# Optimization experiments

Measured on AMD Instinct MI355X. Metric: run time of the kernel, lower is better.

The kernel has to match this reference:

```python
import jax, jax.numpy as jnp
import numpy as np


def setup_inputs() -> dict:
    key = jax.random.key(0)
    k1, k2, k3 = jax.random.split(key, 3)
    B, N, Nq, D, Dv = 32, 4096, 8, 64, 64
    return {
        "keys": jax.random.normal(k1, (B, N, D), dtype=jnp.float32),
        "values": jax.random.normal(k2, (B, N, Dv), dtype=jnp.float32),
        "query": jax.random.normal(k3, (B, Nq, D), dtype=jnp.float32),
    }


def reference(keys, values, query):
    eps = 1e-8
    d = keys.shape[-1]
    # scores: B x N x N'  (same math as broadcast multiply + sum over D)
    alpha = jnp.einsum("bnd,bmd->bnm", keys, query) / jnp.sqrt(jnp.float32(d))
    # softmax over slots (last axis)
    alpha = jax.nn.softmax(alpha, axis=-1) + eps
    # renormalize over input tokens (axis=1)
    alpha = alpha / jnp.sum(alpha, axis=1, keepdims=True)
    # weighted sum of values over N: B x N' x D'
    return jnp.einsum("bnm,bnv->bmv", alpha, values)
```

## Files before the change

### kernel.cpp

```cpp
#include <hip/hip_runtime.h>

#define BB 32
#define NN 4096
#define NQ 8
#define DD 64
#define DV 64
#define CHUNKS 16
#define TOK_PER_BLOCK (NN / CHUNKS)
#define TOK_PER_WAVE (TOK_PER_BLOCK / 4)
#define NGROUP (TOK_PER_WAVE / 8)

template <int CTRL>
__device__ __forceinline__ float dpp_add(float x) {
    union { float f; int i; } in, out;
    in.f = x;
    out.i = __builtin_amdgcn_update_dpp(0, in.i, CTRL, 0xF, 0xF, true);
    return x + out.f;
}
__device__ __forceinline__ float swz16_add(float x) {
    union { float f; int i; } in, out;
    in.f = x;
    out.i = __builtin_amdgcn_ds_swizzle(in.i, 0x401F);
    return x + out.f;
}

__global__ __launch_bounds__(256, 2) void slot_attn_partial(
    const float* __restrict__ keys, const float* __restrict__ values,
    const float* __restrict__ query, float* __restrict__ PU, float* __restrict__ PS)
{
    const int b     = blockIdx.y;
    const int chnk  = blockIdx.x;
    const int tid   = threadIdx.x;
    const int wave  = tid >> 6;
    const int lane  = tid & 63;
    const int t_sub = lane >> 3;
    const int g     = lane & 7;

    float4 q0[8], q1[8];
    const float* qb = query + (size_t)b * NQ * DD + 8 * g;
#pragma unroll
    for (int m = 0; m < 8; ++m) {
        float4 a = *(const float4*)(qb + m * DD);
        float4 c = *(const float4*)(qb + m * DD + 4);
        a.x *= 0.125f; a.y *= 0.125f; a.z *= 0.125f; a.w *= 0.125f;
        c.x *= 0.125f; c.y *= 0.125f; c.z *= 0.125f; c.w *= 0.125f;
        q0[m] = a; q1[m] = c;
    }

    const int tok0 = chnk * TOK_PER_BLOCK + wave * TOK_PER_WAVE;
    const float* Kbase = keys   + ((size_t)b * NN + tok0) * DD + 8 * g;
    const float* Vbase = values + ((size_t)b * NN + tok0) * DV + 8 * g;

    float u[8][8];
#pragma unroll
    for (int m = 0; m < 8; ++m)
#pragma unroll
        for (int j = 0; j < 8; ++j) u[m][j] = 0.f;
    float s_acc[8];
#pragma unroll
    for (int m = 0; m < 8; ++m) s_acc[m] = 0.f;

    float4 kb0[3], kb1[3], vb0[3], vb1[3];
#pragma unroll
    for (int p = 0; p < 2; ++p) {
        const float4* kp = (const float4*)(Kbase + (size_t)(8 * p + t_sub) * DD);
        const float4* vp = (const float4*)(Vbase + (size_t)(8 * p + t_sub) * DV);
        kb0[p] = kp[0]; kb1[p] = kp[1]; vb0[p] = vp[0]; vb1[p] = vp[1];
    }

#pragma unroll
    for (int i = 0; i < NGROUP; ++i) {
        const int cur = i % 3;
        if (i + 2 < NGROUP) {
            const int nxt = (i + 2) % 3;
            const float4* kp = (const float4*)(Kbase + (size_t)(8 * (i + 2) + t_sub) * DD);
            const float4* vp = (const float4*)(Vbase + (size_t)(8 * (i + 2) + t_sub) * DV);
            kb0[nxt] = kp[0]; kb1[nxt] = kp[1]; vb0[nxt] = vp[0]; vb1[nxt] = vp[1];
        }

        const float4 kc0 = kb0[cur], kc1 = kb1[cur];
        float s[8];
#pragma unroll
        for (int m = 0; m < 8; ++m) {
            s[m] = kc0.x * q0[m].x + kc0.y * q0[m].y + kc0.z * q0[m].z + kc0.w * q0[m].w
                 + kc1.x * q1[m].x + kc1.y * q1[m].y + kc1.z * q1[m].z + kc1.w * q1[m].w;
        }
#pragma unroll
        for (int m = 0; m < 8; ++m) {
            s[m] = dpp_add<0xB1>(s[m]);
            s[m] = dpp_add<0x4E>(s[m]);
            s[m] = dpp_add<0x141>(s[m]);
        }
        float e[8], sum = 0.f;
#pragma unroll
        for (int m = 0; m < 8; ++m) { e[m] = __expf(s[m]); sum += e[m]; }
        const float r = __builtin_amdgcn_rcpf(sum);
        const float4 vc0 = vb0[cur], vc1 = vb1[cur];
#pragma unroll
        for (int m = 0; m < 8; ++m) {
            const float a = e[m] * r + 1e-8f;
            s_acc[m] += a;
            u[m][0] += a * vc0.x; u[m][1] += a * vc0.y;
            u[m][2] += a * vc0.z; u[m][3] += a * vc0.w;
            u[m][4] += a * vc1.x; u[m][5] += a * vc1.y;
            u[m][6] += a * vc1.z; u[m][7] += a * vc1.w;
        }
    }

#pragma unroll
    for (int m = 0; m < 8; ++m) {
#pragma unroll
        for (int j = 0; j < 8; ++j) {
            u[m][j] = dpp_add<0x128>(u[m][j]);
            u[m][j] = swz16_add(u[m][j]);
        }
        s_acc[m] = dpp_add<0x128>(s_acc[m]);
        s_acc[m] = swz16_add(s_acc[m]);
    }

    __shared__ float lds[8 * 512];
    __shared__ float lds_s[8 * 8];
    const int half = lane >> 5;
    if ((lane & 24) == 0) {
        float* dst = lds + (wave * 2 + half) * 512 + 8 * g;
#pragma unroll
        for (int m = 0; m < 8; ++m)
#pragma unroll
            for (int j = 0; j < 8; ++j) dst[m * 64 + j] = u[m][j];
        if (g == 0) {
#pragma unroll
            for (int m = 0; m < 8; ++m) lds_s[(wave * 2 + half) * 8 + m] = s_acc[m];
        }
    }
    __syncthreads();

    float* pu = PU + ((size_t)b * CHUNKS + chnk) * 512;
#pragma unroll
    for (int o = 0; o < 2; ++o) {
        int idx = o * 256 + tid;
        float sum = 0.f;
#pragma unroll
        for (int k = 0; k < 8; ++k) sum += lds[k * 512 + idx];
        pu[idx] = sum;
    }
    if (tid < 8) {
        float ssum = 0.f;
#pragma unroll
        for (int k = 0; k < 8; ++k) ssum += lds_s[k * 8 + tid];
        PS[((size_t)b * CHUNKS + chnk) * 8 + tid] = ssum;
    }
}

__global__ __launch_bounds__(512) void slot_attn_reduce(
    const float* __restrict__ PU, const float* __restrict__ PS,
    float* __restrict__ out)
{
    const int b = blockIdx.x;
    const int i = threadIdx.x;

    __shared__ float ssum[NQ];
    if (i < NQ) {
        float s = 0.f;
        const float* ps = PS + (size_t)b * CHUNKS * 8 + i;
#pragma unroll
        for (int c = 0; c < CHUNKS; ++c) s += ps[c * 8];
        ssum[i] = s;
    }
    __syncthreads();

    float usum = 0.f;
    const float* pu = PU + (size_t)b * CHUNKS * 512 + i;
#pragma unroll
    for (int c = 0; c < CHUNKS; ++c) usum += pu[c * 512];
    out[(size_t)b * 512 + i] = usum / ssum[i >> 6];
}

extern "C" void kernel_launch(void* const* d_in, const int* in_sizes, int n_in,
                              void* d_out, int out_size, void* d_ws, size_t ws_size,
                              hipStream_t stream) {
    const float* keys   = (const float*)d_in[0];
    const float* values = (const float*)d_in[1];
    const float* query  = (const float*)d_in[2];
    float* out = (float*)d_out;

    float* PU = (float*)d_ws;
    float* PS = PU + (size_t)BB * CHUNKS * 512;

    slot_attn_partial<<<dim3(CHUNKS, BB), 256, 0, stream>>>(keys, values, query, PU, PS);
    slot_attn_reduce<<<dim3(BB), 512, 0, stream>>>(PU, PS, out);
}
```

Before: 99.45 us.

## Fuse chunk reduction into partial kernel via last-block atomic counter

```diff
diff --git a/kernel.cpp b/kernel.cpp
--- a/kernel.cpp
+++ b/kernel.cpp
@@ -5,7 +5,7 @@
 #define NQ 8
 #define DD 64
 #define DV 64
-#define CHUNKS 16
+#define CHUNKS 32
 #define TOK_PER_BLOCK (NN / CHUNKS)
 #define TOK_PER_WAVE (TOK_PER_BLOCK / 4)
 #define NGROUP (TOK_PER_WAVE / 8)
@@ -24,9 +24,10 @@
     return x + out.f;
 }
 
-__global__ __launch_bounds__(256, 2) void slot_attn_partial(
+__global__ __launch_bounds__(256, 3) void slot_attn_fused(
     const float* __restrict__ keys, const float* __restrict__ values,
-    const float* __restrict__ query, float* __restrict__ PU, float* __restrict__ PS)
+    const float* __restrict__ query, float* __restrict__ PU,
+    float* __restrict__ PS, int* __restrict__ counters, float* __restrict__ out)
 {
     const int b     = blockIdx.y;
     const int chnk  = blockIdx.x;
@@ -60,21 +61,20 @@
 #pragma unroll
     for (int m = 0; m < 8; ++m) s_acc[m] = 0.f;
 
-    float4 kb0[3], kb1[3], vb0[3], vb1[3];
-#pragma unroll
-    for (int p = 0; p < 2; ++p) {
-        const float4* kp = (const float4*)(Kbase + (size_t)(8 * p + t_sub) * DD);
-        const float4* vp = (const float4*)(Vbase + (size_t)(8 * p + t_sub) * DV);
-        kb0[p] = kp[0]; kb1[p] = kp[1]; vb0[p] = vp[0]; vb1[p] = vp[1];
+    float4 kb0[2], kb1[2], vb0[2], vb1[2];
+    {
+        const float4* kp = (const float4*)(Kbase + (size_t)t_sub * DD);
+        const float4* vp = (const float4*)(Vbase + (size_t)t_sub * DV);
+        kb0[0] = kp[0]; kb1[0] = kp[1]; vb0[0] = vp[0]; vb1[0] = vp[1];
     }
 
 #pragma unroll
     for (int i = 0; i < NGROUP; ++i) {
-        const int cur = i % 3;
-        if (i + 2 < NGROUP) {
-            const int nxt = (i + 2) % 3;
-            const float4* kp = (const float4*)(Kbase + (size_t)(8 * (i + 2) + t_sub) * DD);
-            const float4* vp = (const float4*)(Vbase + (size_t)(8 * (i + 2) + t_sub) * DV);
+        const int cur = i & 1;
+        if (i + 1 < NGROUP) {
+            const int nxt = cur ^ 1;
+            const float4* kp = (const float4*)(Kbase + (size_t)(8 * (i + 1) + t_sub) * DD);
+            const float4* vp = (const float4*)(Vbase + (size_t)(8 * (i + 1) + t_sub) * DV);
             kb0[nxt] = kp[0]; kb1[nxt] = kp[1]; vb0[nxt] = vp[0]; vb1[nxt] = vp[1];
         }
 
@@ -149,30 +149,36 @@
         for (int k = 0; k < 8; ++k) ssum += lds_s[k * 8 + tid];
         PS[((size_t)b * CHUNKS + chnk) * 8 + tid] = ssum;
     }
-}
 
-__global__ __launch_bounds__(512) void slot_attn_reduce(
-    const float* __restrict__ PU, const float* __restrict__ PS,
-    float* __restrict__ out)
-{
-    const int b = blockIdx.x;
-    const int i = threadIdx.x;
+    __syncthreads();
+    __shared__ int is_last;
+    if (tid == 0) {
+        __threadfence();
+        is_last = (atomicAdd(&counters[b], 1) == CHUNKS - 1);
+    }
+    __syncthreads();
+    if (!is_last) return;
+    __threadfence();
 
-    __shared__ float ssum[NQ];
-    if (i < NQ) {
+    __shared__ float ssum_f[NQ];
+    if (tid < NQ) {
         float s = 0.f;
-        const float* ps = PS + (size_t)b * CHUNKS * 8 + i;
+        const float* ps = PS + (size_t)b * CHUNKS * 8 + tid;
 #pragma unroll
         for (int c = 0; c < CHUNKS; ++c) s += ps[c * 8];
-        ssum[i] = s;
+        ssum_f[tid] = s;
     }
     __syncthreads();
 
-    float usum = 0.f;
-    const float* pu = PU + (size_t)b * CHUNKS * 512 + i;
+    const float* pub = PU + (size_t)b * CHUNKS * 512;
 #pragma unroll
-    for (int c = 0; c < CHUNKS; ++c) usum += pu[c * 512];
-    out[(size_t)b * 512 + i] = usum / ssum[i >> 6];
+    for (int o = 0; o < 2; ++o) {
+        int idx = o * 256 + tid;
+        float usum = 0.f;
+#pragma unroll
+        for (int c = 0; c < CHUNKS; ++c) usum += pub[c * 512 + idx];
+        out[(size_t)b * 512 + idx] = usum / ssum_f[idx >> 6];
+    }
 }
 
 extern "C" void kernel_launch(void* const* d_in, const int* in_sizes, int n_in,
@@ -185,7 +191,9 @@
 
     float* PU = (float*)d_ws;
     float* PS = PU + (size_t)BB * CHUNKS * 512;
+    int* counters = (int*)(PS + (size_t)BB * CHUNKS * 8);
 
-    slot_attn_partial<<<dim3(CHUNKS, BB), 256, 0, stream>>>(keys, values, query, PU, PS);
-    slot_attn_reduce<<<dim3(BB), 512, 0, stream>>>(PU, PS, out);
+    hipMemsetAsync(counters, 0, BB * sizeof(int), stream);
+    slot_attn_fused<<<dim3(CHUNKS, BB), 256, 0, stream>>>(
+        keys, values, query, PU, PS, counters, out);
 }
```

After: 142.8 us. 1.44x slower.
